# Kernel tuning notes

Hardware: AMD Instinct MI355X
Metric: run time of the kernel (lower is better)

The kernel has to match this reference:

```python
import jax, jax.numpy as jnp
import numpy as np

B, S, V, E, H, C = 64, 1024, 50000, 256, 256, 20
BOUND_P = 0.05  # ~20-word sentences


def setup_inputs() -> dict:
    key = jax.random.key(0)
    k1, k2, k3, k4, k5, k6, k7 = jax.random.split(key, 7)
    tokens = jax.random.randint(k1, (B, S), 2, V)
    is_bound = jax.random.uniform(k2, (B, S)) < BOUND_P
    batch_x = jnp.where(is_bound, 1, tokens)
    batch_x = batch_x.at[:, S - 1].set(1)  # force final sentence boundary
    batch_lens = jnp.full((B,), S, dtype=jnp.int32)
    emb = jax.random.normal(k3, (V, E), dtype=jnp.float32) * 0.1
    W1 = jax.random.normal(k4, (E, H), dtype=jnp.float32) * (1.0 / np.sqrt(E))
    b1 = jnp.zeros((H,), dtype=jnp.float32)
    W2 = jax.random.normal(k5, (H, H), dtype=jnp.float32) * (1.0 / np.sqrt(H))
    b2 = jnp.zeros((H,), dtype=jnp.float32)
    W3 = jax.random.normal(k6, (H, C), dtype=jnp.float32) * (1.0 / np.sqrt(H))
    b3 = jnp.zeros((C,), dtype=jnp.float32)
    return {"batch_x": batch_x, "batch_lens": batch_lens, "emb": emb,
            "W1": W1, "b1": b1, "W2": W2, "b2": b2, "W3": W3, "b3": b3}


def reference(batch_x, batch_lens, emb, W1, b1, W2, b2, W3, b3):
    # word embedding gather: (B,S,E)
    word_embed = emb[batch_x]
    # word2sent nn layer (position-wise fc + tanh), dropout=identity (eval)
    h = jnp.tanh(jnp.einsum('bse,eh->bsh', word_embed, W1) + b1)
    # sentence segmentation: token id 1 marks end of sentence (inclusive)
    is_bound = (batch_x == 1)
    bcum = jnp.cumsum(is_bound.astype(jnp.int32), axis=1)
    local_id = bcum - is_bound.astype(jnp.int32)  # sentence index of each token
    doc_lens = bcum[:, -1]                        # sentences per doc
    valid = local_id < doc_lens[:, None]          # tokens after last boundary dropped
    seg = jnp.arange(B, dtype=jnp.int32)[:, None] * S + local_id
    seg = jnp.where(valid, seg, B * S)            # dump invalid tokens in spare bucket
    h_flat = h.reshape(B * S, H)
    sums = jax.ops.segment_sum(h_flat, seg.reshape(-1), num_segments=B * S + 1)[:B * S]
    cnts = jax.ops.segment_sum(valid.astype(h.dtype).reshape(-1), seg.reshape(-1),
                               num_segments=B * S + 1)[:B * S]
    # word2sent mean pooling (padded/empty slots -> 0, matching F.pad)
    sent_embed = (sums / jnp.maximum(cnts, 1.0)[:, None]).reshape(B, S, H)
    # sent2doc nn layer + mean pooling over valid sentences
    sent_hidden = jnp.tanh(jnp.einsum('bsh,hk->bsk', sent_embed, W2) + b2)
    sent_valid = (jnp.arange(S)[None, :] < doc_lens[:, None]).astype(h.dtype)
    doc_embed = jnp.einsum('bsk,bs->bk', sent_hidden, sent_valid) / doc_lens[:, None].astype(h.dtype)
    # classifier head
    cat_space = doc_embed @ W3 + b3
    return jax.nn.log_softmax(cat_space, axis=-1)
```

## Files before the change

kernel.cpp:

```cpp
#include <hip/hip_runtime.h>
#include <hip/hip_bf16.h>
#include <cstdint>
#include <cstddef>

#define NB 64
#define NS 1024
#define NV 50000
#define NE 256
#define NH 256
#define NC 20
#define MAXSEG 25

typedef short bf16x8 __attribute__((ext_vector_type(8)));
typedef float f32x4 __attribute__((ext_vector_type(4)));

#define WS_W1T    0
#define WS_W2T    131072
#define WS_STARTS 262144
#define WS_LENS   524544
#define WS_PREF   524800
#define WS_PBLK   526848
#define WS_DSUM   13634048

__device__ inline float bf2f(unsigned short u) {
    return __uint_as_float(((unsigned int)u) << 16);
}
__device__ inline unsigned short f2bf(float f) {
    unsigned int x = __float_as_uint(f);
    unsigned int r = (x + 0x7FFFu + ((x >> 16) & 1u)) >> 16;
    return (unsigned short)r;
}
__device__ inline float fast_tanh(float x) {
    float e = __expf(2.f * x);
    return 1.f - 2.f / (e + 1.f);
}

__global__ void setup_kernel(const float* __restrict__ W1, const float* __restrict__ W2,
                             const int* __restrict__ x,
                             unsigned short* __restrict__ W1T, unsigned short* __restrict__ W2T,
                             int* __restrict__ starts, int* __restrict__ lens,
                             int* __restrict__ pref) {
    int blk = blockIdx.x;
    if (blk < 512) {
        int idx = blk * 256 + threadIdx.x;
        if (idx < NE * NH) {
            int h = idx >> 8, e = idx & 255;
            W1T[idx] = f2bf(W1[e * NH + h]);
        } else {
            int i = idx - NE * NH;
            int j = i >> 8, k = i & 255;
            W2T[i] = f2bf(W2[k * NH + j]);
        }
    } else {
        if (threadIdx.x >= 64) return;
        int b = blk - 512;
        int lane = threadIdx.x;
        const int* row = x + b * NS;
        int* st = starts + b * (NS + 1);
        if (lane == 0) st[0] = 0;
        int cnt = 0;
        for (int it = 0; it < NS / 64; ++it) {
            if ((it & 1) == 0 && lane == 0) pref[b * 8 + (it >> 1)] = cnt;
            int s = it * 64 + lane;
            bool isb = (row[s] == 1);
            unsigned long long bal = __ballot(isb);
            int pre = __popcll(bal & ((1ull << lane) - 1ull));
            if (isb) st[cnt + pre + 1] = s + 1;
            cnt += __popcll(bal);
        }
        if (lane == 0) lens[b] = cnt;
    }
}

__global__ __launch_bounds__(512, 2) void gemm1_kernel(
    const int* __restrict__ batch_x, const float* __restrict__ emb,
    const unsigned short* __restrict__ W1T, const float* __restrict__ b1,
    float* __restrict__ pblk)
{
    __shared__ unsigned short As[2][16][264];
    __shared__ unsigned short Hs[16][264];
    __shared__ int sidtab[128];

    int tid = threadIdx.x;
    int lane = tid & 63;
    int w = tid >> 6;
    int lr = lane & 15;
    int g = lane >> 4;
    int kb0 = g * 8;
    int base = blockIdx.x * 128;

    if (w == 0) {
        int cnt = 0;
        #pragma unroll
        for (int c = 0; c < 2; ++c) {
            int t = c * 64 + lane;
            bool isb = (batch_x[base + t] == 1);
            unsigned long long bal = __ballot(isb);
            int pre = __popcll(bal & ((1ull << lane) - 1ull));
            int sid = cnt + pre;
            sidtab[t] = sid < MAXSEG ? sid : MAXSEG - 1;
            cnt += __popcll(bal);
        }
    }

    bf16x8 Bf[16];
    #pragma unroll
    for (int ks = 0; ks < 8; ++ks)
        #pragma unroll
        for (int n = 0; n < 2; ++n)
            Bf[ks * 2 + n] = *reinterpret_cast<const bf16x8*>(
                W1T + (size_t)(w * 32 + n * 16 + lr) * NE + ks * 32 + kb0);
    float bb[2];
    #pragma unroll
    for (int n = 0; n < 2; ++n) bb[n] = b1[w * 32 + n * 16 + lr];

    float4 gr[2];
    #pragma unroll
    for (int i = 0; i < 2; ++i) {
        int f = tid + i * 512;
        int row = f >> 6, c4 = (f & 63) * 4;
        int xv = batch_x[base + row];
        gr[i] = *reinterpret_cast<const float4*>(emb + (size_t)xv * NE + c4);
    }
    #pragma unroll
    for (int i = 0; i < 2; ++i) {
        int f = tid + i * 512;
        int row = f >> 6, c4 = (f & 63) * 4;
        ushort4 u;
        u.x = f2bf(gr[i].x); u.y = f2bf(gr[i].y); u.z = f2bf(gr[i].z); u.w = f2bf(gr[i].w);
        *reinterpret_cast<ushort4*>(&As[0][row][c4]) = u;
    }

    int cur_sid = 0;
    float running = 0.f;

    for (int t = 0; t < 8; ++t) {
        __syncthreads();
        int cur = t & 1;

        if (t + 1 < 8) {
            #pragma unroll
            for (int i = 0; i < 2; ++i) {
                int f = tid + i * 512;
                int row = f >> 6, c4 = (f & 63) * 4;
                int xv = batch_x[base + (t + 1) * 16 + row];
                gr[i] = *reinterpret_cast<const float4*>(emb + (size_t)xv * NE + c4);
            }
        }

        f32x4 acc[2];
        #pragma unroll
        for (int n = 0; n < 2; ++n) acc[n] = (f32x4){0.f, 0.f, 0.f, 0.f};
        #pragma unroll
        for (int ks = 0; ks < 8; ++ks) {
            bf16x8 a = *reinterpret_cast<const bf16x8*>(&As[cur][lr][ks * 32 + kb0]);
            #pragma unroll
            for (int n = 0; n < 2; ++n)
                acc[n] = __builtin_amdgcn_mfma_f32_16x16x32_bf16(a, Bf[ks * 2 + n], acc[n], 0, 0, 0);
        }

        #pragma unroll
        for (int n = 0; n < 2; ++n) {
            int col = w * 32 + n * 16 + lr;
            #pragma unroll
            for (int j = 0; j < 4; ++j)
                Hs[g * 4 + j][col] = f2bf(fast_tanh(acc[n][j] + bb[n]));
        }
        __syncthreads();

        if (tid < 256) {
            int rowbase = t * 16;
            #pragma unroll
            for (int r = 0; r < 16; ++r) {
                int s = sidtab[rowbase + r];
                if (s != cur_sid) {
                    pblk[((size_t)blockIdx.x * MAXSEG + cur_sid) * NH + tid] = running;
                    running = 0.f; cur_sid = s;
                }
                running += bf2f(Hs[r][tid]);
            }
        }

        if (t + 1 < 8) {
            #pragma unroll
            for (int i = 0; i < 2; ++i) {
                int f = tid + i * 512;
                int row = f >> 6, c4 = (f & 63) * 4;
                ushort4 u;
                u.x = f2bf(gr[i].x); u.y = f2bf(gr[i].y); u.z = f2bf(gr[i].z); u.w = f2bf(gr[i].w);
                *reinterpret_cast<ushort4*>(&As[cur ^ 1][row][c4]) = u;
            }
        }
    }
    if (tid < 256)
        pblk[((size_t)blockIdx.x * MAXSEG + cur_sid) * NH + tid] = running;
}

__global__ __launch_bounds__(256, 2) void sgemm_kernel(
    const float* __restrict__ pblk, const int* __restrict__ starts,
    const int* __restrict__ lens, const int* __restrict__ pref,
    const unsigned short* __restrict__ W2T, const float* __restrict__ b2,
    float* __restrict__ dsum)
{
    int b = blockIdx.y;
    int t = blockIdx.x;
    int i0 = t * 16;
    int L = lens[b];
    if (i0 >= L) return;

    int tid = threadIdx.x;
    int lane = tid & 63;
    int w = tid >> 6;
    int lr = lane & 15;
    int g = lane >> 4;
    int kb0 = g * 8;

    __shared__ unsigned short ms[16][264];
    bf16x8 Bf[32];
    #pragma unroll
    for (int ks = 0; ks < 8; ++ks)
        #pragma unroll
        for (int n = 0; n < 4; ++n)
            Bf[ks * 4 + n] = *reinterpret_cast<const bf16x8*>(
                W2T + (size_t)(w * 64 + n * 16 + lr) * NH + ks * 32 + kb0);
    float bb[4];
    #pragma unroll
    for (int n = 0; n < 4; ++n) bb[n] = b2[w * 64 + n * 16 + lr];

    const int* st = starts + b * (NS + 1);
    for (int s = 0; s < 16; ++s) {
        int i = i0 + s;
        float m = 0.f;
        if (i < L) {
            int s0 = st[i], e0 = st[i + 1];
            int tb1 = (e0 - 1) >> 7;
            float sum = 0.f;
            for (int tb = s0 >> 7; tb <= tb1; ++tb) {
                int blk = b * 8 + tb;
                sum += pblk[((size_t)blk * MAXSEG + (i - pref[blk])) * NH + tid];
            }
            m = sum / (float)(e0 - s0);
        }
        ms[s][tid] = f2bf(m);
    }
    __syncthreads();

    f32x4 acc[4];
    #pragma unroll
    for (int n = 0; n < 4; ++n) acc[n] = (f32x4){0.f, 0.f, 0.f, 0.f};
    #pragma unroll
    for (int ks = 0; ks < 8; ++ks) {
        bf16x8 a = *reinterpret_cast<const bf16x8*>(&ms[lr][ks * 32 + kb0]);
        #pragma unroll
        for (int n = 0; n < 4; ++n)
            acc[n] = __builtin_amdgcn_mfma_f32_16x16x32_bf16(a, Bf[ks * 4 + n], acc[n], 0, 0, 0);
    }

    float* dp = dsum + ((size_t)b * 8 + t) * NH;
    #pragma unroll
    for (int n = 0; n < 4; ++n) {
        float v = 0.f;
        #pragma unroll
        for (int j = 0; j < 4; ++j) {
            int srow = i0 + g * 4 + j;
            float hv = tanhf(acc[n][j] + bb[n]);
            v += (srow < L) ? hv : 0.f;
        }
        v += __shfl_xor(v, 16, 64);
        v += __shfl_xor(v, 32, 64);
        if (g == 0) dp[w * 64 + n * 16 + lr] = v;
    }
}

__global__ __launch_bounds__(256) void doc_kernel(
    const float* __restrict__ dsum, const int* __restrict__ lens,
    const float* __restrict__ W3, const float* __restrict__ b3,
    float* __restrict__ out)
{
    int b = blockIdx.x;
    int j = threadIdx.x;
    int L = lens[b];
    int ntiles = (L + 15) >> 4;

    float s = 0.f;
    for (int t = 0; t < ntiles; ++t)
        s += dsum[((size_t)b * 8 + t) * NH + j];

    __shared__ float d[NH];
    d[j] = s / (float)L;
    __syncthreads();

    __shared__ float cat[NC];
    if (j < NC) {
        float a = b3[j];
        #pragma unroll 8
        for (int k = 0; k < NH; ++k) a += d[k] * W3[k * NC + j];
        cat[j] = a;
    }
    __syncthreads();

    if (j == 0) {
        float mx = -1e30f;
        for (int c = 0; c < NC; ++c) mx = fmaxf(mx, cat[c]);
        float se = 0.f;
        for (int c = 0; c < NC; ++c) se += expf(cat[c] - mx);
        float lse = logf(se) + mx;
        for (int c = 0; c < NC; ++c) out[b * NC + c] = cat[c] - lse;
    }
}

extern "C" void kernel_launch(void* const* d_in, const int* in_sizes, int n_in,
                              void* d_out, int out_size, void* d_ws, size_t ws_size,
                              hipStream_t stream) {
    const int*   batch_x = (const int*)d_in[0];
    const float* emb = (const float*)d_in[2];
    const float* W1  = (const float*)d_in[3];
    const float* b1  = (const float*)d_in[4];
    const float* W2  = (const float*)d_in[5];
    const float* b2  = (const float*)d_in[6];
    const float* W3  = (const float*)d_in[7];
    const float* b3  = (const float*)d_in[8];
    float* out = (float*)d_out;

    char* ws = (char*)d_ws;
    unsigned short* W1T   = (unsigned short*)(ws + WS_W1T);
    unsigned short* W2T   = (unsigned short*)(ws + WS_W2T);
    int*            starts= (int*)(ws + WS_STARTS);
    int*            lens  = (int*)(ws + WS_LENS);
    int*            pref  = (int*)(ws + WS_PREF);
    float*          pblk  = (float*)(ws + WS_PBLK);
    float*          dsum  = (float*)(ws + WS_DSUM);

    hipLaunchKernelGGL(setup_kernel, dim3(512 + NB), dim3(256), 0, stream,
                       W1, W2, batch_x, W1T, W2T, starts, lens, pref);
    hipLaunchKernelGGL(gemm1_kernel, dim3((NB * NS) / 128), dim3(512), 0, stream,
                       batch_x, emb, W1T, b1, pblk);
    hipLaunchKernelGGL(sgemm_kernel, dim3(8, NB), dim3(256), 0, stream,
                       pblk, starts, lens, pref, W2T, b2, dsum);
    hipLaunchKernelGGL(doc_kernel, dim3(NB), dim3(256), 0, stream,
                       dsum, lens, W3, b3, out);
}
```

Measured before the change: 71.94 us.

## Triple-buffer gemm1 gather and segment-reduce MFMA outputs in registers via shuffles

The gemm1 kernel now prefetches embedding rows two tiles ahead into alternating register sets and uses a three-slot LDS ring. This removes one of the two block barriers per iteration. The bf16 Hs staging buffer is gone: each wave masks its MFMA outputs per sentence, reduces across lane groups with xor-shuffles, and accumulates running sums in registers. This cuts LDS traffic and a sync, and it also stops rounding h to bf16 before pooling. The cost is more registers and a shuffle loop that runs once per segment in each tile.

```diff
diff --git a/kernel.cpp b/kernel.cpp
--- a/kernel.cpp
+++ b/kernel.cpp
@@ -5,7 +5,6 @@
 
 #define NB 64
 #define NS 1024
-#define NV 50000
 #define NE 256
 #define NH 256
 #define NC 20
@@ -77,8 +76,7 @@
     const unsigned short* __restrict__ W1T, const float* __restrict__ b1,
     float* __restrict__ pblk)
 {
-    __shared__ unsigned short As[2][16][264];
-    __shared__ unsigned short Hs[16][264];
+    __shared__ unsigned short As[3][16][264];
     __shared__ int sidtab[128];
 
     int tid = threadIdx.x;
@@ -89,17 +87,20 @@
     int kb0 = g * 8;
     int base = blockIdx.x * 128;
 
+    int r0 = tid >> 6,          c0 = (tid & 63) * 4;
+    int r1 = (tid + 512) >> 6,  c1 = c0;
+
     if (w == 0) {
-        int cnt = 0;
+        int cc = 0;
         #pragma unroll
         for (int c = 0; c < 2; ++c) {
             int t = c * 64 + lane;
             bool isb = (batch_x[base + t] == 1);
             unsigned long long bal = __ballot(isb);
             int pre = __popcll(bal & ((1ull << lane) - 1ull));
-            int sid = cnt + pre;
+            int sid = cc + pre;
             sidtab[t] = sid < MAXSEG ? sid : MAXSEG - 1;
-            cnt += __popcll(bal);
+            cc += __popcll(bal);
         }
     }
 
@@ -114,38 +115,38 @@
     #pragma unroll
     for (int n = 0; n < 2; ++n) bb[n] = b1[w * 32 + n * 16 + lr];
 
-    float4 gr[2];
-    #pragma unroll
-    for (int i = 0; i < 2; ++i) {
-        int f = tid + i * 512;
-        int row = f >> 6, c4 = (f & 63) * 4;
-        int xv = batch_x[base + row];
-        gr[i] = *reinterpret_cast<const float4*>(emb + (size_t)xv * NE + c4);
-    }
-    #pragma unroll
-    for (int i = 0; i < 2; ++i) {
-        int f = tid + i * 512;
-        int row = f >> 6, c4 = (f & 63) * 4;
-        ushort4 u;
-        u.x = f2bf(gr[i].x); u.y = f2bf(gr[i].y); u.z = f2bf(gr[i].z); u.w = f2bf(gr[i].w);
-        *reinterpret_cast<ushort4*>(&As[0][row][c4]) = u;
+    float4 grA[2], grB[2];
+    {
+        int xv0 = batch_x[base + r0];
+        int xv1 = batch_x[base + r1];
+        grA[0] = *reinterpret_cast<const float4*>(emb + (size_t)xv0 * NE + c0);
+        grA[1] = *reinterpret_cast<const float4*>(emb + (size_t)xv1 * NE + c1);
+        int yv0 = batch_x[base + 16 + r0];
+        int yv1 = batch_x[base + 16 + r1];
+        grB[0] = *reinterpret_cast<const float4*>(emb + (size_t)yv0 * NE + c0);
+        grB[1] = *reinterpret_cast<const float4*>(emb + (size_t)yv1 * NE + c1);
+    }
+    {
+        ushort4 u0, u1;
+        u0.x = f2bf(grA[0].x); u0.y = f2bf(grA[0].y); u0.z = f2bf(grA[0].z); u0.w = f2bf(grA[0].w);
+        u1.x = f2bf(grA[1].x); u1.y = f2bf(grA[1].y); u1.z = f2bf(grA[1].z); u1.w = f2bf(grA[1].w);
+        *reinterpret_cast<ushort4*>(&As[0][r0][c0]) = u0;
+        *reinterpret_cast<ushort4*>(&As[0][r1][c1]) = u1;
     }
 
     int cur_sid = 0;
-    float running = 0.f;
+    float run0 = 0.f, run1 = 0.f;
+    size_t blkoff = (size_t)blockIdx.x * MAXSEG * NH;
 
     for (int t = 0; t < 8; ++t) {
         __syncthreads();
-        int cur = t & 1;
-
-        if (t + 1 < 8) {
-            #pragma unroll
-            for (int i = 0; i < 2; ++i) {
-                int f = tid + i * 512;
-                int row = f >> 6, c4 = (f & 63) * 4;
-                int xv = batch_x[base + (t + 1) * 16 + row];
-                gr[i] = *reinterpret_cast<const float4*>(emb + (size_t)xv * NE + c4);
-            }
+
+        if (t + 2 < 8) {
+            float4* gd = (t & 1) ? grB : grA;
+            int xv0 = batch_x[base + (t + 2) * 16 + r0];
+            int xv1 = batch_x[base + (t + 2) * 16 + r1];
+            gd[0] = *reinterpret_cast<const float4*>(emb + (size_t)xv0 * NE + c0);
+            gd[1] = *reinterpret_cast<const float4*>(emb + (size_t)xv1 * NE + c1);
         }
 
         f32x4 acc[2];
@@ -153,47 +154,60 @@
         for (int n = 0; n < 2; ++n) acc[n] = (f32x4){0.f, 0.f, 0.f, 0.f};
         #pragma unroll
         for (int ks = 0; ks < 8; ++ks) {
-            bf16x8 a = *reinterpret_cast<const bf16x8*>(&As[cur][lr][ks * 32 + kb0]);
+            bf16x8 a = *reinterpret_cast<const bf16x8*>(&As[t % 3][lr][ks * 32 + kb0]);
             #pragma unroll
             for (int n = 0; n < 2; ++n)
                 acc[n] = __builtin_amdgcn_mfma_f32_16x16x32_bf16(a, Bf[ks * 2 + n], acc[n], 0, 0, 0);
         }
 
-        #pragma unroll
-        for (int n = 0; n < 2; ++n) {
-            int col = w * 32 + n * 16 + lr;
+        if (t + 1 < 8) {
+            float4* gs = ((t + 1) & 1) ? grB : grA;
+            ushort4 u0, u1;
+            u0.x = f2bf(gs[0].x); u0.y = f2bf(gs[0].y); u0.z = f2bf(gs[0].z); u0.w = f2bf(gs[0].w);
+            u1.x = f2bf(gs[1].x); u1.y = f2bf(gs[1].y); u1.z = f2bf(gs[1].z); u1.w = f2bf(gs[1].w);
+            *reinterpret_cast<ushort4*>(&As[(t + 1) % 3][r0][c0]) = u0;
+            *reinterpret_cast<ushort4*>(&As[(t + 1) % 3][r1][c1]) = u1;
+        }
+
+        float h[2][4];
+        #pragma unroll
+        for (int n = 0; n < 2; ++n)
             #pragma unroll
             for (int j = 0; j < 4; ++j)
-                Hs[g * 4 + j][col] = f2bf(fast_tanh(acc[n][j] + bb[n]));
-        }
-        __syncthreads();
-
-        if (tid < 256) {
-            int rowbase = t * 16;
+                h[n][j] = fast_tanh(acc[n][j] + bb[n]);
+
+        int tb = t * 16;
+        int sbase = sidtab[tb];
+        int nseg = sidtab[tb + 15] - sbase + 1;
+        int sid_[4];
+        #pragma unroll
+        for (int j = 0; j < 4; ++j) sid_[j] = sidtab[tb + g * 4 + j];
+
+        for (int s = 0; s < nseg; ++s) {
+            int gs2 = sbase + s;
+            float v0 = 0.f, v1 = 0.f;
             #pragma unroll
-            for (int r = 0; r < 16; ++r) {
-                int s = sidtab[rowbase + r];
-                if (s != cur_sid) {
-                    pblk[((size_t)blockIdx.x * MAXSEG + cur_sid) * NH + tid] = running;
-                    running = 0.f; cur_sid = s;
+            for (int j = 0; j < 4; ++j) {
+                bool m = (sid_[j] == gs2);
+                v0 += m ? h[0][j] : 0.f;
+                v1 += m ? h[1][j] : 0.f;
+            }
+            v0 += __shfl_xor(v0, 16, 64); v0 += __shfl_xor(v0, 32, 64);
+            v1 += __shfl_xor(v1, 16, 64); v1 += __shfl_xor(v1, 32, 64);
+            if (gs2 != cur_sid) {
+                if (g == 0) {
+                    pblk[blkoff + (size_t)cur_sid * NH + (w * 32 + lr)]      = run0;
+                    pblk[blkoff + (size_t)cur_sid * NH + (w * 32 + 16 + lr)] = run1;
                 }
-                running += bf2f(Hs[r][tid]);
+                run0 = 0.f; run1 = 0.f; cur_sid = gs2;
             }
-        }
-
-        if (t + 1 < 8) {
-            #pragma unroll
-            for (int i = 0; i < 2; ++i) {
-                int f = tid + i * 512;
-                int row = f >> 6, c4 = (f & 63) * 4;
-                ushort4 u;
-                u.x = f2bf(gr[i].x); u.y = f2bf(gr[i].y); u.z = f2bf(gr[i].z); u.w = f2bf(gr[i].w);
-                *reinterpret_cast<ushort4*>(&As[cur ^ 1][row][c4]) = u;
-            }
-        }
-    }
-    if (tid < 256)
-        pblk[((size_t)blockIdx.x * MAXSEG + cur_sid) * NH + tid] = running;
+            run0 += v0; run1 += v1;
+        }
+    }
+    if (g == 0) {
+        pblk[blkoff + (size_t)cur_sid * NH + (w * 32 + lr)]      = run0;
+        pblk[blkoff + (size_t)cur_sid * NH + (w * 32 + 16 + lr)] = run1;
+    }
 }
 
 __global__ __launch_bounds__(256, 2) void sgemm_kernel(
```

After: 82.74 us. 1.15x slower.
